# Kernel optimization log

Measured on AMD Instinct MI355X. Metric: run time of the kernel, lower is better.

The kernel has to match this reference:

```python
import jax, jax.numpy as jnp
import numpy as np

NEG = 0.01  # LeakyReLU negative_slope
N_NODES = 100000
N_EDGES = 400000
D = 128
IN_CH = 16
EDGE_DIM = 1


def _linear(x, w, b):
    # torch.nn.Linear convention: y = x @ W^T + b, W: [out, in]
    return x @ w.T + b


def setup_inputs() -> dict:
    key = jax.random.key(0)
    ks = jax.random.split(key, 32)

    def W(k, o, i):
        return jax.random.normal(k, (o, i), dtype=jnp.float32) * 0.02

    def B(k, o):
        return jax.random.normal(k, (o,), dtype=jnp.float32) * 0.02

    return {
        "x": jax.random.normal(ks[0], (N_NODES, IN_CH), dtype=jnp.float32),
        "edge_index": jax.random.randint(ks[1], (2, N_EDGES), 0, N_NODES, dtype=jnp.int64),
        "edge_weight": jax.random.uniform(ks[2], (N_EDGES, EDGE_DIM), dtype=jnp.float32),
        # prep MLP: in_ch -> 128 (LeakyReLU) -> 128 (Tanh)
        "prep_w0": W(ks[3], D, IN_CH), "prep_b0": B(ks[4], D),
        "prep_w1": W(ks[5], D, D), "prep_b1": B(ks[6], D),
        # GINEConv edge lin: edge_dim -> 128
        "edge_w": W(ks[7], D, EDGE_DIM), "edge_b": B(ks[8], D),
        # GINEConv nn: 128 -> 128 (LReLU) -> 128 (LReLU) -> 128 (Tanh)
        "mlp_w0": W(ks[9], D, D), "mlp_b0": B(ks[10], D),
        "mlp_w1": W(ks[11], D, D), "mlp_b1": B(ks[12], D),
        "mlp_w2": W(ks[13], D, D), "mlp_b2": B(ks[14], D),
        # post MLP: (128+128) -> 128 (LReLU) -> 64 (Tanh)
        "post_w0": W(ks[15], D, 2 * D), "post_b0": B(ks[16], D),
        "post_w1": W(ks[17], 64, D), "post_b1": B(ks[18], 64),
    }


def reference(x, edge_index, edge_weight,
              prep_w0, prep_b0, prep_w1, prep_b1,
              edge_w, edge_b,
              mlp_w0, mlp_b0, mlp_w1, mlp_b1, mlp_w2, mlp_b2,
              post_w0, post_b0, post_w1, post_b1):
    lrelu = lambda v: jax.nn.leaky_relu(v, negative_slope=NEG)
    n = x.shape[0]

    # sequential_prep
    h = lrelu(_linear(x, prep_w0, prep_b0))
    h = jnp.tanh(_linear(h, prep_w1, prep_b1))  # [N, D]

    r = h  # skip connection (x.clone())

    # GINEConv: message = relu(x_j + lin(edge_attr)); aggr = sum per dst
    e = _linear(edge_weight, edge_w, edge_b)            # [E, D]
    m = jax.nn.relu(h[edge_index[0]] + e)               # gather + edge add
    agg = jax.ops.segment_sum(m, edge_index[1], num_segments=n)  # scatter-sum
    z = h + agg  # (1 + eps) * x_i + aggr, eps = 0
    z = lrelu(_linear(z, mlp_w0, mlp_b0))
    z = lrelu(_linear(z, mlp_w1, mlp_b1))
    z = jnp.tanh(_linear(z, mlp_w2, mlp_b2))            # [N, D]

    # skip-cat
    h2 = jnp.concatenate([z, r], axis=1)                # [N, 2D]

    # sequential_post
    o = lrelu(_linear(h2, post_w0, post_b0))
    o = jnp.tanh(_linear(o, post_w1, post_b1))          # [N, 64]
    return o
```

## Files before the change

### kernel.cpp

```cpp
#include <hip/hip_runtime.h>

typedef short bf16x8 __attribute__((ext_vector_type(8)));
typedef float f32x4 __attribute__((ext_vector_type(4)));

#define NEG 0.01f

#define OFF_P0  0
#define OFF_P1  8192
#define OFF_M0  40960
#define OFF_Q0A 139264
#define OFF_Q0B 172032
#define OFF_Q1  204800
#define WBF_BYTES 221184

#define VMCNT0 asm volatile("s_waitcnt vmcnt(0)" ::: "memory")
#define LGKM0  asm volatile("s_waitcnt lgkmcnt(0)" ::: "memory")

__device__ __forceinline__ unsigned short f2bf(float f) {
  union { float f; unsigned u; } v; v.f = f;
  unsigned u = v.u;
  return (unsigned short)((u + 0x7fffu + ((u >> 16) & 1u)) >> 16);
}
__device__ __forceinline__ unsigned pack2(float a, float b) {
  return ((unsigned)f2bf(b) << 16) | (unsigned)f2bf(a);
}
__device__ __forceinline__ float bflo(unsigned u) { return __uint_as_float(u << 16); }
__device__ __forceinline__ float bfhi(unsigned u) { return __uint_as_float(u & 0xffff0000u); }
__device__ __forceinline__ float lrelu(float v) { return fmaxf(v, 0.0f) + NEG * fminf(v, 0.0f); }
__device__ __forceinline__ float tanh_fast(float x) {
  float e = __expf(2.0f * x);
  return 1.0f - __fdividef(2.0f, e + 1.0f);
}

__device__ __forceinline__ void gll16(const void* g, void* l) {
  __builtin_amdgcn_global_load_lds((const __attribute__((address_space(1))) void*)g,
                                   (__attribute__((address_space(3))) void*)l, 16, 0, 0);
}

__device__ __forceinline__ void gll_lin(const char* g, char* l, int nchunks, int wv, int nw, int lane) {
  for (int j = wv; j < nchunks; j += nw)
    gll16(g + j * 1024 + lane * 16, l + j * 1024 + lane * 16);
}

__device__ __forceinline__ void gll_rows(const char* gsrc, char* scr, int strip, int N, int lane) {
  #pragma unroll
  for (int c = 0; c < 8; ++c) {
    int L = c * 1024 + lane * 16;
    int row = strip + (L >> 8);
    row = row < N ? row : N - 1;
    gll16(gsrc + (size_t)row * 256 + (L & 255), scr + c * 1024 + lane * 16);
  }
}

__device__ __forceinline__ void copy_rows_out(const char* scr, char* gdst, int strip, int N, int lane) {
  #pragma unroll
  for (int c = 0; c < 8; ++c) {
    int L = c * 1024 + lane * 16;
    int row = strip + (L >> 8);
    if (row < N) *(uint4*)(gdst + (size_t)strip * 256 + L) = *(const uint4*)(scr + L);
  }
}

__device__ __forceinline__ void zacc82(f32x4 acc[8][2]) {
  #pragma unroll
  for (int m = 0; m < 8; ++m)
    #pragma unroll
    for (int n = 0; n < 2; ++n) { f32x4 z = {0.f,0.f,0.f,0.f}; acc[m][n] = z; }
}

__device__ __forceinline__ void gemm128(const char* wbase, const bf16x8 b[2][4],
                                        f32x4 acc[8][2], int l15, int lg) {
  #pragma unroll
  for (int ks = 0; ks < 4; ++ks)
    #pragma unroll
    for (int mf = 0; mf < 8; ++mf) {
      const int row = 16*mf + l15;
      bf16x8 a = *(const bf16x8*)(wbase + row*256 + ((16*lg + 64*ks) ^ ((row&7)<<4)));
      acc[mf][0] = __builtin_amdgcn_mfma_f32_16x16x32_bf16(a, b[0][ks], acc[mf][0], 0,0,0);
      acc[mf][1] = __builtin_amdgcn_mfma_f32_16x16x32_bf16(a, b[1][ks], acc[mf][1], 0,0,0);
    }
}

__device__ __forceinline__ void read_bfrags(const char* scr, bf16x8 b[2][4], int l15, int lg) {
  #pragma unroll
  for (int nf = 0; nf < 2; ++nf) {
    const int n = 16*nf + l15;
    #pragma unroll
    for (int ks = 0; ks < 4; ++ks)
      b[nf][ks] = *(const bf16x8*)(scr + n*256 + ((16*lg + 64*ks) ^ ((n&7)<<4)));
  }
}

template<int ACT>
__device__ __forceinline__ void ep_lds(const f32x4 acc[8][2], const float* __restrict__ bias,
                                       char* scr, int l15, int lg) {
  #pragma unroll
  for (int mf = 0; mf < 8; ++mf) {
    const int ch4 = 16*mf + 4*lg;
    const float4 bv = *(const float4*)(bias + ch4);
    #pragma unroll
    for (int nf = 0; nf < 2; ++nf) {
      const int n = 16*nf + l15;
      float v0 = acc[mf][nf][0]+bv.x, v1 = acc[mf][nf][1]+bv.y;
      float v2 = acc[mf][nf][2]+bv.z, v3 = acc[mf][nf][3]+bv.w;
      if (ACT == 0) { v0=lrelu(v0); v1=lrelu(v1); v2=lrelu(v2); v3=lrelu(v3); }
      else { v0=tanh_fast(v0); v1=tanh_fast(v1); v2=tanh_fast(v2); v3=tanh_fast(v3); }
      uint2 o = { pack2(v0,v1), pack2(v2,v3) };
      *(uint2*)(scr + n*256 + ((32*mf + 8*lg) ^ ((n&7)<<4))) = o;
    }
  }
}

extern "C" __global__ void __launch_bounds__(256) wpack_kernel(
    const float* __restrict__ pw0, const float* __restrict__ pw1,
    const float* __restrict__ mw0, const float* __restrict__ mw1, const float* __restrict__ mw2,
    const float* __restrict__ qw0, const float* __restrict__ qw1,
    char* wbf, int* deg, int N) {
  int gid = blockIdx.x * 256 + threadIdx.x;
  if (gid < 13824) {
    int c = gid;
    const float* src = nullptr;
    int dstB = 0;
    bool zero = false;
    if (c < 512) { int r = c >> 2, q = c & 3;
      dstB = OFF_P0 + r*64 + ((q*16) ^ ((r&3)<<4));
      if (q < 2) src = pw0 + r*16 + q*8; else zero = true;
    } else if (c < 2560) { int i = c - 512, r = i >> 4, q = i & 15;
      dstB = OFF_P1 + r*256 + ((q*16) ^ ((r&7)<<4));
      src = pw1 + r*128 + q*8;
    } else if (c < 8704) { int i = c - 2560, sl = i >> 11, j = i & 2047, r = j >> 4, q = j & 15;
      const float* m = (sl==0) ? mw0 : ((sl==1) ? mw1 : mw2);
      dstB = OFF_M0 + sl*32768 + r*256 + ((q*16) ^ ((r&7)<<4));
      src = m + r*128 + q*8;
    } else if (c < 10752) { int i = c - 8704, r = i >> 4, q = i & 15;
      dstB = OFF_Q0A + r*256 + ((q*16) ^ ((r&7)<<4));
      src = qw0 + r*256 + q*8;
    } else if (c < 12800) { int i = c - 10752, r = i >> 4, q = i & 15;
      dstB = OFF_Q0B + r*256 + ((q*16) ^ ((r&7)<<4));
      src = qw0 + r*256 + 128 + q*8;
    } else { int i = c - 12800, r = i >> 4, q = i & 15;
      dstB = OFF_Q1 + r*256 + ((q*16) ^ ((r&7)<<4));
      src = qw1 + r*128 + q*8;
    }
    ushort4 lo, hi;
    if (zero) { lo.x=lo.y=lo.z=lo.w=0; hi.x=hi.y=hi.z=hi.w=0; }
    else {
      float4 a = *(const float4*)src, b = *(const float4*)(src + 4);
      lo.x=f2bf(a.x); lo.y=f2bf(a.y); lo.z=f2bf(a.z); lo.w=f2bf(a.w);
      hi.x=f2bf(b.x); hi.y=f2bf(b.y); hi.z=f2bf(b.z); hi.w=f2bf(b.w);
    }
    *(ushort4*)(wbf + dstB) = lo;
    *(ushort4*)(wbf + dstB + 8) = hi;
  }
  if (gid < N) deg[gid] = 0;
}

extern "C" __global__ void __launch_bounds__(512) prep_kernel(
    const float* __restrict__ x,
    const float* __restrict__ pb0, const float* __restrict__ pb1,
    const char* __restrict__ wbf,
    const int* __restrict__ ei, int* deg, int E,
    char* hB, int N, int ntiles) {
  __shared__ char wP[40960];
  __shared__ char xw_all[8 * 2048];
  __shared__ char scr_all[8 * 8192];
  const int tid = threadIdx.x, lane = tid & 63, wv = tid >> 6;
  const int l15 = lane & 15, lg = lane >> 4;

  gll_lin(wbf + OFF_P0, wP, 40, wv, 8, lane);
  for (int e = blockIdx.x*512 + tid; e < E; e += gridDim.x*512)
    atomicAdd(&deg[ei[E + e]], 1);
  VMCNT0; __syncthreads();

  char* xw  = xw_all  + wv * 2048;
  char* scr = scr_all + wv * 8192;
  const char* xc = (const char*)x;

  for (int tile = blockIdx.x; tile < ntiles; tile += gridDim.x) {
    const int strip = tile*256 + wv*32;
    LGKM0;
    #pragma unroll
    for (int c = 0; c < 2; ++c) {
      int L = c*1024 + lane*16;
      int row = strip + (L >> 6);
      row = row < N ? row : N - 1;
      gll16(xc + (size_t)row*64 + (L & 63), xw + c*1024 + lane*16);
    }
    VMCNT0;
    bf16x8 bx[2];
    #pragma unroll
    for (int nf = 0; nf < 2; ++nf) {
      const int n = 16*nf + l15;
      if (lg < 2) {
        float4 u = *(const float4*)(xw + n*64 + lg*32);
        float4 v = *(const float4*)(xw + n*64 + lg*32 + 16);
        bf16x8 t;
        t[0]=(short)f2bf(u.x); t[1]=(short)f2bf(u.y); t[2]=(short)f2bf(u.z); t[3]=(short)f2bf(u.w);
        t[4]=(short)f2bf(v.x); t[5]=(short)f2bf(v.y); t[6]=(short)f2bf(v.z); t[7]=(short)f2bf(v.w);
        bx[nf] = t;
      } else {
        bf16x8 t = {0,0,0,0,0,0,0,0}; bx[nf] = t;
      }
    }
    f32x4 acc[8][2];
    zacc82(acc);
    #pragma unroll
    for (int mf = 0; mf < 8; ++mf) {
      const int row = 16*mf + l15;
      bf16x8 a = *(const bf16x8*)(wP + row*64 + ((16*lg) ^ ((row&3)<<4)));
      acc[mf][0] = __builtin_amdgcn_mfma_f32_16x16x32_bf16(a, bx[0], acc[mf][0], 0,0,0);
      acc[mf][1] = __builtin_amdgcn_mfma_f32_16x16x32_bf16(a, bx[1], acc[mf][1], 0,0,0);
    }
    ep_lds<0>(acc, pb0, scr, l15, lg);
    bf16x8 b1[2][4];
    read_bfrags(scr, b1, l15, lg);
    zacc82(acc);
    gemm128(wP + 8192, b1, acc, l15, lg);
    ep_lds<1>(acc, pb1, scr, l15, lg);
    copy_rows_out(scr, hB, strip, N, lane);
  }
}

extern "C" __global__ void __launch_bounds__(256) scan_partials_kernel(
    const int* __restrict__ deg, int* partials, int N) {
  __shared__ int red[256];
  int b = blockIdx.x, t = threadIdx.x;
  int base = b * 2048 + t * 8, s = 0;
  #pragma unroll
  for (int i = 0; i < 8; ++i) { int idx = base + i; s += (idx < N) ? deg[idx] : 0; }
  red[t] = s; __syncthreads();
  for (int off = 128; off > 0; off >>= 1) {
    if (t < off) red[t] += red[t + off];
    __syncthreads();
  }
  if (t == 0) partials[b] = red[0];
}

extern "C" __global__ void scan_base_kernel(const int* __restrict__ partials, int* basearr, int nb) {
  int lane = threadIdx.x;
  int orig = (lane < nb) ? partials[lane] : 0;
  int v = orig;
  #pragma unroll
  for (int off = 1; off < 64; off <<= 1) {
    int u = __shfl_up(v, off);
    if (lane >= off) v += u;
  }
  if (lane < nb) basearr[lane] = v - orig;
}

extern "C" __global__ void __launch_bounds__(256) scan_apply_kernel(
    const int* __restrict__ deg, const int* __restrict__ basearr,
    int* offs, int* cur, int N) {
  __shared__ int sc[256];
  int b = blockIdx.x, t = threadIdx.x;
  int base = b * 2048 + t * 8;
  int loc[8], s = 0;
  #pragma unroll
  for (int i = 0; i < 8; ++i) { int idx = base + i; loc[i] = (idx < N) ? deg[idx] : 0; s += loc[i]; }
  sc[t] = s; __syncthreads();
  for (int off = 1; off < 256; off <<= 1) {
    int v = sc[t];
    int u = (t >= off) ? sc[t - off] : 0;
    __syncthreads();
    sc[t] = v + u;
    __syncthreads();
  }
  int run = basearr[b] + ((t == 0) ? 0 : sc[t - 1]);
  #pragma unroll
  for (int i = 0; i < 8; ++i) {
    int idx = base + i;
    if (idx < N) { offs[idx] = run; cur[idx] = run; run += loc[i]; }
  }
}

extern "C" __global__ void __launch_bounds__(256) scatter_kernel(
    const int* __restrict__ ei, const float* __restrict__ ew,
    int* cur, int2* recs, int E) {
  int e = blockIdx.x * 256 + threadIdx.x;
  if (e < E) {
    int dst = ei[E + e];
    int slot = atomicAdd(&cur[dst], 1);
    int2 r; r.x = ei[e]; r.y = __float_as_int(ew[e]);
    recs[slot] = r;
  }
}

extern "C" __global__ void __launch_bounds__(256) agg_kernel(
    const int* __restrict__ offs, const int* __restrict__ cur,
    const int2* __restrict__ recs,
    const float* __restrict__ elw, const float* __restrict__ elb,
    const char* __restrict__ hB, char* zB, int N) {
  const int lane = threadIdx.x & 63, wv = threadIdx.x >> 6;
  const int node = blockIdx.x * 4 + wv;
  if (node >= N) return;
  const float2 wl = *(const float2*)(elw + 2*lane);
  const float2 bl = *(const float2*)(elb + 2*lane);
  const int byteL = lane * 4;
  const int s = offs[node], e = cur[node];
  float c0 = 0.f, c1 = 0.f;
  int j = s;
  for (; j + 4 <= e; j += 4) {
    int2 r0 = recs[j], r1 = recs[j+1], r2 = recs[j+2], r3 = recs[j+3];
    unsigned u0 = *(const unsigned*)(hB + (size_t)r0.x*256 + (byteL ^ ((r0.x&7)<<4)));
    unsigned u1 = *(const unsigned*)(hB + (size_t)r1.x*256 + (byteL ^ ((r1.x&7)<<4)));
    unsigned u2 = *(const unsigned*)(hB + (size_t)r2.x*256 + (byteL ^ ((r2.x&7)<<4)));
    unsigned u3 = *(const unsigned*)(hB + (size_t)r3.x*256 + (byteL ^ ((r3.x&7)<<4)));
    float w0 = __int_as_float(r0.y), w1 = __int_as_float(r1.y);
    float w2 = __int_as_float(r2.y), w3 = __int_as_float(r3.y);
    c0 += fmaxf(bflo(u0) + w0*wl.x + bl.x, 0.f); c1 += fmaxf(bfhi(u0) + w0*wl.y + bl.y, 0.f);
    c0 += fmaxf(bflo(u1) + w1*wl.x + bl.x, 0.f); c1 += fmaxf(bfhi(u1) + w1*wl.y + bl.y, 0.f);
    c0 += fmaxf(bflo(u2) + w2*wl.x + bl.x, 0.f); c1 += fmaxf(bfhi(u2) + w2*wl.y + bl.y, 0.f);
    c0 += fmaxf(bflo(u3) + w3*wl.x + bl.x, 0.f); c1 += fmaxf(bfhi(u3) + w3*wl.y + bl.y, 0.f);
  }
  for (; j < e; ++j) {
    int2 r = recs[j];
    unsigned u = *(const unsigned*)(hB + (size_t)r.x*256 + (byteL ^ ((r.x&7)<<4)));
    float w = __int_as_float(r.y);
    c0 += fmaxf(bflo(u) + w*wl.x + bl.x, 0.f);
    c1 += fmaxf(bfhi(u) + w*wl.y + bl.y, 0.f);
  }
  unsigned hs = *(const unsigned*)(hB + (size_t)node*256 + (byteL ^ ((node&7)<<4)));
  unsigned o = pack2(bflo(hs) + c0, bfhi(hs) + c1);
  *(unsigned*)(zB + (size_t)node*256 + (byteL ^ ((node&7)<<4))) = o;
}

extern "C" __global__ void __launch_bounds__(384) nodeA_kernel(
    const char* __restrict__ zB, const char* __restrict__ wbf,
    const float* __restrict__ mb0, const float* __restrict__ mb1, const float* __restrict__ mb2,
    char* z3, int N, int ntiles) {
  __shared__ char wM[98304];
  __shared__ char scrA[6 * 8192];
  const int tid = threadIdx.x, lane = tid & 63, wv = tid >> 6;
  const int l15 = lane & 15, lg = lane >> 4;

  gll_lin(wbf + OFF_M0, wM, 96, wv, 6, lane);
  VMCNT0; __syncthreads();
  char* scr = scrA + wv * 8192;

  for (int tile = blockIdx.x; tile < ntiles; tile += gridDim.x) {
    const int strip = tile*192 + wv*32;
    LGKM0;
    gll_rows(zB, scr, strip, N, lane);
    VMCNT0;
    bf16x8 b0[2][4];
    read_bfrags(scr, b0, l15, lg);
    f32x4 acc[8][2];
    zacc82(acc);
    gemm128(wM, b0, acc, l15, lg);
    ep_lds<0>(acc, mb0, scr, l15, lg);
    bf16x8 b1[2][4];
    read_bfrags(scr, b1, l15, lg);
    zacc82(acc);
    gemm128(wM + 32768, b1, acc, l15, lg);
    ep_lds<0>(acc, mb1, scr, l15, lg);
    bf16x8 b2[2][4];
    read_bfrags(scr, b2, l15, lg);
    zacc82(acc);
    gemm128(wM + 65536, b2, acc, l15, lg);
    ep_lds<1>(acc, mb2, scr, l15, lg);
    copy_rows_out(scr, z3, strip, N, lane);
  }
}

extern "C" __global__ void __launch_bounds__(384) nodeB_kernel(
    const char* __restrict__ z3, const char* __restrict__ hB, const char* __restrict__ wbf,
    const float* __restrict__ qb0, const float* __restrict__ qb1,
    float* out, int N, int ntiles) {
  __shared__ char wQ[81920];
  __shared__ char scrB[6 * 8192];
  const int tid = threadIdx.x, lane = tid & 63, wv = tid >> 6;
  const int l15 = lane & 15, lg = lane >> 4;

  gll_lin(wbf + OFF_Q0A, wQ, 80, wv, 6, lane);
  VMCNT0; __syncthreads();
  char* scr = scrB + wv * 8192;

  for (int tile = blockIdx.x; tile < ntiles; tile += gridDim.x) {
    const int strip = tile*192 + wv*32;
    LGKM0;
    gll_rows(z3, scr, strip, N, lane);
    VMCNT0;
    bf16x8 bz[2][4];
    read_bfrags(scr, bz, l15, lg);
    LGKM0;
    gll_rows(hB, scr, strip, N, lane);
    f32x4 acc[8][2];
    zacc82(acc);
    gemm128(wQ, bz, acc, l15, lg);
    VMCNT0;
    bf16x8 bh[2][4];
    read_bfrags(scr, bh, l15, lg);
    gemm128(wQ + 32768, bh, acc, l15, lg);
    ep_lds<0>(acc, qb0, scr, l15, lg);
    bf16x8 bt[2][4];
    read_bfrags(scr, bt, l15, lg);
    f32x4 a2[4][2];
    #pragma unroll
    for (int m = 0; m < 4; ++m)
      #pragma unroll
      for (int n = 0; n < 2; ++n) { f32x4 z = {0.f,0.f,0.f,0.f}; a2[m][n] = z; }
    #pragma unroll
    for (int ks = 0; ks < 4; ++ks)
      #pragma unroll
      for (int mf = 0; mf < 4; ++mf) {
        const int row = 16*mf + l15;
        bf16x8 a = *(const bf16x8*)(wQ + 65536 + row*256 + ((16*lg + 64*ks) ^ ((row&7)<<4)));
        a2[mf][0] = __builtin_amdgcn_mfma_f32_16x16x32_bf16(a, bt[0][ks], a2[mf][0], 0,0,0);
        a2[mf][1] = __builtin_amdgcn_mfma_f32_16x16x32_bf16(a, bt[1][ks], a2[mf][1], 0,0,0);
      }
    #pragma unroll
    for (int mf = 0; mf < 4; ++mf) {
      const int ch4 = 16*mf + 4*lg;
      const float4 bv = *(const float4*)(qb1 + ch4);
      #pragma unroll
      for (int nf = 0; nf < 2; ++nf) {
        const int node = strip + 16*nf + l15;
        if (node < N) {
          float4 o;
          o.x = tanh_fast(a2[mf][nf][0] + bv.x);
          o.y = tanh_fast(a2[mf][nf][1] + bv.y);
          o.z = tanh_fast(a2[mf][nf][2] + bv.z);
          o.w = tanh_fast(a2[mf][nf][3] + bv.w);
          *(float4*)(out + (size_t)node*64 + ch4) = o;
        }
      }
    }
  }
}

extern "C" void kernel_launch(void* const* d_in, const int* in_sizes, int n_in,
                              void* d_out, int out_size, void* d_ws, size_t ws_size,
                              hipStream_t stream) {
  const float* x   = (const float*)d_in[0];
  const int*   ei  = (const int*)d_in[1];
  const float* ew  = (const float*)d_in[2];
  const float* pw0 = (const float*)d_in[3];
  const float* pb0 = (const float*)d_in[4];
  const float* pw1 = (const float*)d_in[5];
  const float* pb1 = (const float*)d_in[6];
  const float* elw = (const float*)d_in[7];
  const float* elb = (const float*)d_in[8];
  const float* mw0 = (const float*)d_in[9];
  const float* mb0 = (const float*)d_in[10];
  const float* mw1 = (const float*)d_in[11];
  const float* mb1 = (const float*)d_in[12];
  const float* mw2 = (const float*)d_in[13];
  const float* mb2 = (const float*)d_in[14];
  const float* qw0 = (const float*)d_in[15];
  const float* qb0 = (const float*)d_in[16];
  const float* qw1 = (const float*)d_in[17];
  const float* qb1 = (const float*)d_in[18];
  float* out = (float*)d_out;

  const int N = in_sizes[0] / 16;
  const int E = in_sizes[1] / 2;

  char* p = (char*)d_ws;
  auto alloc = [&](size_t bytes) { char* r = p; p += (bytes + 255) & ~(size_t)255; return r; };
  const size_t rowBytes = (size_t)N * 256;

  char* zB      = alloc(rowBytes);
  char* z3      = alloc(rowBytes);
  int2* recs    = (int2*)alloc((size_t)E * 8);
  int*  deg     = (int*)alloc((size_t)N * 4);
  int*  offs    = (int*)alloc((size_t)N * 4);
  int*  cur     = (int*)alloc((size_t)N * 4);
  int*  part    = (int*)alloc(256 * 4);
  int*  basearr = (int*)alloc(256 * 4);
  char* wbf     = alloc(WBF_BYTES);

  char* hB;
  if ((size_t)(p - (char*)d_ws) + rowBytes <= ws_size) {
    hB = alloc(rowBytes);
  } else {
    hB = (char*)d_out;
  }

  const int ntilesP  = (N + 255) / 256;
  const int ntilesAB = (N + 191) / 192;
  const int nb1  = (N + 2047) / 2048;
  const int eblk = (E + 255) / 256;
  const int pgrid = ((13824 > N ? 13824 : N) + 255) / 256;

  wpack_kernel<<<dim3(pgrid), dim3(256), 0, stream>>>(pw0, pw1, mw0, mw1, mw2, qw0, qw1,
                                                      wbf, deg, N);
  prep_kernel<<<dim3(256), dim3(512), 0, stream>>>(x, pb0, pb1, wbf, ei, deg, E, hB, N, ntilesP);
  scan_partials_kernel<<<dim3(nb1), dim3(256), 0, stream>>>(deg, part, N);
  scan_base_kernel<<<dim3(1), dim3(64), 0, stream>>>(part, basearr, nb1);
  scan_apply_kernel<<<dim3(nb1), dim3(256), 0, stream>>>(deg, basearr, offs, cur, N);
  scatter_kernel<<<dim3(eblk), dim3(256), 0, stream>>>(ei, ew, cur, recs, E);
  agg_kernel<<<dim3((N + 3) / 4), dim3(256), 0, stream>>>(offs, cur, recs, elw, elb, hB, zB, N);
  nodeA_kernel<<<dim3(256), dim3(384), 0, stream>>>(zB, wbf, mb0, mb1, mb2, z3, N, ntilesAB);
  nodeB_kernel<<<dim3(256), dim3(384), 0, stream>>>(z3, hB, wbf, qb0, qb1, out, N, ntilesAB);
}
```

Baseline: 278.5 us.

## Fuse node MLP kernels, single-block CSR scan, read weights from global

Merges nodeA and nodeB into one node kernel so the z3 intermediate is never written to or read back from global memory. The three scan kernels are replaced by one 1024-thread single-block scan. The prep and node kernels now use one 256-node tile per block instead of persistent loops, and read weight fragments straight from global/L2 instead of staging them in LDS. This frees LDS for two blocks per CU, at the cost of repeated global weight reads and a serial single-block scan.

```diff
diff --git a/kernel.cpp b/kernel.cpp
--- a/kernel.cpp
+++ b/kernel.cpp
@@ -14,7 +14,6 @@
 #define WBF_BYTES 221184
 
 #define VMCNT0 asm volatile("s_waitcnt vmcnt(0)" ::: "memory")
-#define LGKM0  asm volatile("s_waitcnt lgkmcnt(0)" ::: "memory")
 
 __device__ __forceinline__ unsigned short f2bf(float f) {
   union { float f; unsigned u; } v; v.f = f;
@@ -35,11 +34,6 @@
 __device__ __forceinline__ void gll16(const void* g, void* l) {
   __builtin_amdgcn_global_load_lds((const __attribute__((address_space(1))) void*)g,
                                    (__attribute__((address_space(3))) void*)l, 16, 0, 0);
-}
-
-__device__ __forceinline__ void gll_lin(const char* g, char* l, int nchunks, int wv, int nw, int lane) {
-  for (int j = wv; j < nchunks; j += nw)
-    gll16(g + j * 1024 + lane * 16, l + j * 1024 + lane * 16);
 }
 
 __device__ __forceinline__ void gll_rows(const char* gsrc, char* scr, int strip, int N, int lane) {
@@ -155,121 +149,88 @@
   if (gid < N) deg[gid] = 0;
 }
 
-extern "C" __global__ void __launch_bounds__(512) prep_kernel(
+extern "C" __global__ void __launch_bounds__(512, 2) prep_kernel(
     const float* __restrict__ x,
     const float* __restrict__ pb0, const float* __restrict__ pb1,
     const char* __restrict__ wbf,
     const int* __restrict__ ei, int* deg, int E,
-    char* hB, int N, int ntiles) {
-  __shared__ char wP[40960];
-  __shared__ char xw_all[8 * 2048];
+    char* hB, int N) {
   __shared__ char scr_all[8 * 8192];
   const int tid = threadIdx.x, lane = tid & 63, wv = tid >> 6;
   const int l15 = lane & 15, lg = lane >> 4;
-
-  gll_lin(wbf + OFF_P0, wP, 40, wv, 8, lane);
+  char* scr = scr_all + wv * 8192;
+
   for (int e = blockIdx.x*512 + tid; e < E; e += gridDim.x*512)
     atomicAdd(&deg[ei[E + e]], 1);
-  VMCNT0; __syncthreads();
-
-  char* xw  = xw_all  + wv * 2048;
-  char* scr = scr_all + wv * 8192;
-  const char* xc = (const char*)x;
-
-  for (int tile = blockIdx.x; tile < ntiles; tile += gridDim.x) {
-    const int strip = tile*256 + wv*32;
-    LGKM0;
-    #pragma unroll
-    for (int c = 0; c < 2; ++c) {
-      int L = c*1024 + lane*16;
-      int row = strip + (L >> 6);
-      row = row < N ? row : N - 1;
-      gll16(xc + (size_t)row*64 + (L & 63), xw + c*1024 + lane*16);
-    }
-    VMCNT0;
-    bf16x8 bx[2];
-    #pragma unroll
-    for (int nf = 0; nf < 2; ++nf) {
-      const int n = 16*nf + l15;
-      if (lg < 2) {
-        float4 u = *(const float4*)(xw + n*64 + lg*32);
-        float4 v = *(const float4*)(xw + n*64 + lg*32 + 16);
-        bf16x8 t;
-        t[0]=(short)f2bf(u.x); t[1]=(short)f2bf(u.y); t[2]=(short)f2bf(u.z); t[3]=(short)f2bf(u.w);
-        t[4]=(short)f2bf(v.x); t[5]=(short)f2bf(v.y); t[6]=(short)f2bf(v.z); t[7]=(short)f2bf(v.w);
-        bx[nf] = t;
-      } else {
-        bf16x8 t = {0,0,0,0,0,0,0,0}; bx[nf] = t;
-      }
-    }
-    f32x4 acc[8][2];
-    zacc82(acc);
-    #pragma unroll
-    for (int mf = 0; mf < 8; ++mf) {
-      const int row = 16*mf + l15;
-      bf16x8 a = *(const bf16x8*)(wP + row*64 + ((16*lg) ^ ((row&3)<<4)));
-      acc[mf][0] = __builtin_amdgcn_mfma_f32_16x16x32_bf16(a, bx[0], acc[mf][0], 0,0,0);
-      acc[mf][1] = __builtin_amdgcn_mfma_f32_16x16x32_bf16(a, bx[1], acc[mf][1], 0,0,0);
-    }
-    ep_lds<0>(acc, pb0, scr, l15, lg);
-    bf16x8 b1[2][4];
-    read_bfrags(scr, b1, l15, lg);
-    zacc82(acc);
-    gemm128(wP + 8192, b1, acc, l15, lg);
-    ep_lds<1>(acc, pb1, scr, l15, lg);
-    copy_rows_out(scr, hB, strip, N, lane);
-  }
-}
-
-extern "C" __global__ void __launch_bounds__(256) scan_partials_kernel(
-    const int* __restrict__ deg, int* partials, int N) {
-  __shared__ int red[256];
-  int b = blockIdx.x, t = threadIdx.x;
-  int base = b * 2048 + t * 8, s = 0;
-  #pragma unroll
-  for (int i = 0; i < 8; ++i) { int idx = base + i; s += (idx < N) ? deg[idx] : 0; }
-  red[t] = s; __syncthreads();
-  for (int off = 128; off > 0; off >>= 1) {
-    if (t < off) red[t] += red[t + off];
+
+  const int strip = blockIdx.x*256 + wv*32;
+  if (strip >= N) return;
+
+  bf16x8 bx[2];
+  #pragma unroll
+  for (int nf = 0; nf < 2; ++nf) {
+    int node = strip + 16*nf + l15; node = node < N ? node : N-1;
+    if (lg < 2) {
+      float4 u = *(const float4*)(x + (size_t)node*16 + lg*8);
+      float4 v = *(const float4*)(x + (size_t)node*16 + lg*8 + 4);
+      bf16x8 t;
+      t[0]=(short)f2bf(u.x); t[1]=(short)f2bf(u.y); t[2]=(short)f2bf(u.z); t[3]=(short)f2bf(u.w);
+      t[4]=(short)f2bf(v.x); t[5]=(short)f2bf(v.y); t[6]=(short)f2bf(v.z); t[7]=(short)f2bf(v.w);
+      bx[nf] = t;
+    } else {
+      bf16x8 t = {0,0,0,0,0,0,0,0}; bx[nf] = t;
+    }
+  }
+  f32x4 acc[8][2];
+  zacc82(acc);
+  #pragma unroll
+  for (int mf = 0; mf < 8; ++mf) {
+    const int row = 16*mf + l15;
+    bf16x8 a = *(const bf16x8*)(wbf + OFF_P0 + row*64 + ((16*lg) ^ ((row&3)<<4)));
+    acc[mf][0] = __builtin_amdgcn_mfma_f32_16x16x32_bf16(a, bx[0], acc[mf][0], 0,0,0);
+    acc[mf][1] = __builtin_amdgcn_mfma_f32_16x16x32_bf16(a, bx[1], acc[mf][1], 0,0,0);
+  }
+  ep_lds<0>(acc, pb0, scr, l15, lg);
+  bf16x8 b1[2][4];
+  read_bfrags(scr, b1, l15, lg);
+  zacc82(acc);
+  gemm128(wbf + OFF_P1, b1, acc, l15, lg);
+  ep_lds<1>(acc, pb1, scr, l15, lg);
+  copy_rows_out(scr, hB, strip, N, lane);
+}
+
+extern "C" __global__ void __launch_bounds__(1024) csr_kernel(
+    const int* __restrict__ deg, int* offs, int* cur, int N) {
+  __shared__ int sums[1024];
+  const int t = threadIdx.x;
+  const int i0 = t * 128;
+  int s = 0;
+  if (i0 < N) {
+    int lim = (i0 + 128 < N) ? i0 + 128 : N;
+    int i = i0;
+    for (; i + 4 <= lim; i += 4) { int4 d = *(const int4*)(deg + i); s += d.x + d.y + d.z + d.w; }
+    for (; i < lim; ++i) s += deg[i];
+  }
+  sums[t] = s;
+  __syncthreads();
+  for (int off = 1; off < 1024; off <<= 1) {
+    int v = sums[t];
+    int u = (t >= off) ? sums[t - off] : 0;
     __syncthreads();
-  }
-  if (t == 0) partials[b] = red[0];
-}
-
-extern "C" __global__ void scan_base_kernel(const int* __restrict__ partials, int* basearr, int nb) {
-  int lane = threadIdx.x;
-  int orig = (lane < nb) ? partials[lane] : 0;
-  int v = orig;
-  #pragma unroll
-  for (int off = 1; off < 64; off <<= 1) {
-    int u = __shfl_up(v, off);
-    if (lane >= off) v += u;
-  }
-  if (lane < nb) basearr[lane] = v - orig;
-}
-
-extern "C" __global__ void __launch_bounds__(256) scan_apply_kernel(
-    const int* __restrict__ deg, const int* __restrict__ basearr,
-    int* offs, int* cur, int N) {
-  __shared__ int sc[256];
-  int b = blockIdx.x, t = threadIdx.x;
-  int base = b * 2048 + t * 8;
-  int loc[8], s = 0;
-  #pragma unroll
-  for (int i = 0; i < 8; ++i) { int idx = base + i; loc[i] = (idx < N) ? deg[idx] : 0; s += loc[i]; }
-  sc[t] = s; __syncthreads();
-  for (int off = 1; off < 256; off <<= 1) {
-    int v = sc[t];
-    int u = (t >= off) ? sc[t - off] : 0;
+    sums[t] = v + u;
     __syncthreads();
-    sc[t] = v + u;
-    __syncthreads();
-  }
-  int run = basearr[b] + ((t == 0) ? 0 : sc[t - 1]);
-  #pragma unroll
-  for (int i = 0; i < 8; ++i) {
-    int idx = base + i;
-    if (idx < N) { offs[idx] = run; cur[idx] = run; run += loc[i]; }
+  }
+  int run = (t == 0) ? 0 : sums[t - 1];
+  if (i0 < N) {
+    int lim = (i0 + 128 < N) ? i0 + 128 : N;
+    int i = i0;
+    for (; i + 4 <= lim; i += 4) {
+      int4 d = *(const int4*)(deg + i);
+      int4 o; o.x = run; o.y = run + d.x; o.z = o.y + d.y; o.w = o.z + d.z;
+      *(int4*)(offs + i) = o; *(int4*)(cur + i) = o;
+      run = o.w + d.w;
+    }
+    for (; i < lim; ++i) { offs[i] = run; cur[i] = run; run += deg[i]; }
   }
 }
 
@@ -324,105 +285,88 @@
   *(unsigned*)(zB + (size_t)node*256 + (byteL ^ ((node&7)<<4))) = o;
 }
 
-extern "C" __global__ void __launch_bounds__(384) nodeA_kernel(
-    const char* __restrict__ zB, const char* __restrict__ wbf,
+extern "C" __global__ void __launch_bounds__(512, 2) node_kernel(
+    const char* __restrict__ zB, const char* hB, const char* __restrict__ wbf,
     const float* __restrict__ mb0, const float* __restrict__ mb1, const float* __restrict__ mb2,
-    char* z3, int N, int ntiles) {
-  __shared__ char wM[98304];
-  __shared__ char scrA[6 * 8192];
+    const float* __restrict__ qb0, const float* __restrict__ qb1,
+    float* out, int N) {
+  __shared__ char scr_all[8 * 8192];
   const int tid = threadIdx.x, lane = tid & 63, wv = tid >> 6;
   const int l15 = lane & 15, lg = lane >> 4;
-
-  gll_lin(wbf + OFF_M0, wM, 96, wv, 6, lane);
-  VMCNT0; __syncthreads();
-  char* scr = scrA + wv * 8192;
-
-  for (int tile = blockIdx.x; tile < ntiles; tile += gridDim.x) {
-    const int strip = tile*192 + wv*32;
-    LGKM0;
-    gll_rows(zB, scr, strip, N, lane);
-    VMCNT0;
-    bf16x8 b0[2][4];
-    read_bfrags(scr, b0, l15, lg);
-    f32x4 acc[8][2];
-    zacc82(acc);
-    gemm128(wM, b0, acc, l15, lg);
-    ep_lds<0>(acc, mb0, scr, l15, lg);
-    bf16x8 b1[2][4];
-    read_bfrags(scr, b1, l15, lg);
-    zacc82(acc);
-    gemm128(wM + 32768, b1, acc, l15, lg);
-    ep_lds<0>(acc, mb1, scr, l15, lg);
-    bf16x8 b2[2][4];
-    read_bfrags(scr, b2, l15, lg);
-    zacc82(acc);
-    gemm128(wM + 65536, b2, acc, l15, lg);
-    ep_lds<1>(acc, mb2, scr, l15, lg);
-    copy_rows_out(scr, z3, strip, N, lane);
-  }
-}
-
-extern "C" __global__ void __launch_bounds__(384) nodeB_kernel(
-    const char* __restrict__ z3, const char* __restrict__ hB, const char* __restrict__ wbf,
-    const float* __restrict__ qb0, const float* __restrict__ qb1,
-    float* out, int N, int ntiles) {
-  __shared__ char wQ[81920];
-  __shared__ char scrB[6 * 8192];
-  const int tid = threadIdx.x, lane = tid & 63, wv = tid >> 6;
-  const int l15 = lane & 15, lg = lane >> 4;
-
-  gll_lin(wbf + OFF_Q0A, wQ, 80, wv, 6, lane);
-  VMCNT0; __syncthreads();
-  char* scr = scrB + wv * 8192;
-
-  for (int tile = blockIdx.x; tile < ntiles; tile += gridDim.x) {
-    const int strip = tile*192 + wv*32;
-    LGKM0;
-    gll_rows(z3, scr, strip, N, lane);
-    VMCNT0;
-    bf16x8 bz[2][4];
-    read_bfrags(scr, bz, l15, lg);
-    LGKM0;
-    gll_rows(hB, scr, strip, N, lane);
-    f32x4 acc[8][2];
-    zacc82(acc);
-    gemm128(wQ, bz, acc, l15, lg);
-    VMCNT0;
-    bf16x8 bh[2][4];
-    read_bfrags(scr, bh, l15, lg);
-    gemm128(wQ + 32768, bh, acc, l15, lg);
-    ep_lds<0>(acc, qb0, scr, l15, lg);
-    bf16x8 bt[2][4];
-    read_bfrags(scr, bt, l15, lg);
-    f32x4 a2[4][2];
-    #pragma unroll
-    for (int m = 0; m < 4; ++m)
-      #pragma unroll
-      for (int n = 0; n < 2; ++n) { f32x4 z = {0.f,0.f,0.f,0.f}; a2[m][n] = z; }
+  char* scr = scr_all + wv * 8192;
+
+  const int strip = blockIdx.x*256 + wv*32;
+  if (strip >= N) return;
+
+  gll_rows(zB, scr, strip, N, lane);
+  VMCNT0;
+
+  bf16x8 b0[2][4];
+  read_bfrags(scr, b0, l15, lg);
+  f32x4 acc[8][2];
+  zacc82(acc);
+  gemm128(wbf + OFF_M0, b0, acc, l15, lg);
+  ep_lds<0>(acc, mb0, scr, l15, lg);
+
+  bf16x8 b1[2][4];
+  read_bfrags(scr, b1, l15, lg);
+  zacc82(acc);
+  gemm128(wbf + OFF_M0 + 32768, b1, acc, l15, lg);
+  ep_lds<0>(acc, mb1, scr, l15, lg);
+
+  bf16x8 b2[2][4];
+  read_bfrags(scr, b2, l15, lg);
+  zacc82(acc);
+  gemm128(wbf + OFF_M0 + 65536, b2, acc, l15, lg);
+  ep_lds<1>(acc, mb2, scr, l15, lg);
+
+  bf16x8 bz[2][4];
+  read_bfrags(scr, bz, l15, lg);
+  bf16x8 bh[2][4];
+  #pragma unroll
+  for (int nf = 0; nf < 2; ++nf) {
+    int node = strip + 16*nf + l15; node = node < N ? node : N-1;
+    const char* hr = hB + (size_t)node*256;
+    const int sw = (node&7) << 4;
     #pragma unroll
     for (int ks = 0; ks < 4; ++ks)
-      #pragma unroll
-      for (int mf = 0; mf < 4; ++mf) {
-        const int row = 16*mf + l15;
-        bf16x8 a = *(const bf16x8*)(wQ + 65536 + row*256 + ((16*lg + 64*ks) ^ ((row&7)<<4)));
-        a2[mf][0] = __builtin_amdgcn_mfma_f32_16x16x32_bf16(a, bt[0][ks], a2[mf][0], 0,0,0);
-        a2[mf][1] = __builtin_amdgcn_mfma_f32_16x16x32_bf16(a, bt[1][ks], a2[mf][1], 0,0,0);
-      }
+      bh[nf][ks] = *(const bf16x8*)(hr + ((16*lg + 64*ks) ^ sw));
+  }
+  zacc82(acc);
+  gemm128(wbf + OFF_Q0A, bz, acc, l15, lg);
+  gemm128(wbf + OFF_Q0B, bh, acc, l15, lg);
+  ep_lds<0>(acc, qb0, scr, l15, lg);
+
+  bf16x8 bt[2][4];
+  read_bfrags(scr, bt, l15, lg);
+  f32x4 a2[4][2];
+  #pragma unroll
+  for (int m = 0; m < 4; ++m)
+    #pragma unroll
+    for (int n = 0; n < 2; ++n) { f32x4 z = {0.f,0.f,0.f,0.f}; a2[m][n] = z; }
+  #pragma unroll
+  for (int ks = 0; ks < 4; ++ks)
     #pragma unroll
     for (int mf = 0; mf < 4; ++mf) {
-      const int ch4 = 16*mf + 4*lg;
-      const float4 bv = *(const float4*)(qb1 + ch4);
-      #pragma unroll
-      for (int nf = 0; nf < 2; ++nf) {
-        const int node = strip + 16*nf + l15;
-        if (node < N) {
-          float4 o;
-          o.x = tanh_fast(a2[mf][nf][0] + bv.x);
-          o.y = tanh_fast(a2[mf][nf][1] + bv.y);
-          o.z = tanh_fast(a2[mf][nf][2] + bv.z);
-          o.w = tanh_fast(a2[mf][nf][3] + bv.w);
-          *(float4*)(out + (size_t)node*64 + ch4) = o;
-        }
+      const int row = 16*mf + l15;
+      bf16x8 a = *(const bf16x8*)(wbf + OFF_Q1 + row*256 + ((16*lg + 64*ks) ^ ((row&7)<<4)));
+      a2[mf][0] = __builtin_amdgcn_mfma_f32_16x16x32_bf16(a, bt[0][ks], a2[mf][0], 0,0,0);
+      a2[mf][1] = __builtin_amdgcn_mfma_f32_16x16x32_bf16(a, bt[1][ks], a2[mf][1], 0,0,0);
+    }
+  #pragma unroll
+  for (int mf = 0; mf < 4; ++mf) {
+    const int ch4 = 16*mf + 4*lg;
+    const float4 bv = *(const float4*)(qb1 + ch4);
+    #pragma unroll
+    for (int nf = 0; nf < 2; ++nf) {
+      const int node = strip + 16*nf + l15;
+      if (node < N) {
+        float4 o;
+        o.x = tanh_fast(a2[mf][nf][0] + bv.x);
+        o.y = tanh_fast(a2[mf][nf][1] + bv.y);
+        o.z = tanh_fast(a2[mf][nf][2] + bv.z);
+        o.w = tanh_fast(a2[mf][nf][3] + bv.w);
+        *(float4*)(out + (size_t)node*64 + ch4) = o;
       }
     }
   }
@@ -460,13 +404,10 @@
   const size_t rowBytes = (size_t)N * 256;
 
   char* zB      = alloc(rowBytes);
-  char* z3      = alloc(rowBytes);
   int2* recs    = (int2*)alloc((size_t)E * 8);
   int*  deg     = (int*)alloc((size_t)N * 4);
   int*  offs    = (int*)alloc((size_t)N * 4);
   int*  cur     = (int*)alloc((size_t)N * 4);
-  int*  part    = (int*)alloc(256 * 4);
-  int*  basearr = (int*)alloc(256 * 4);
   char* wbf     = alloc(WBF_BYTES);
 
   char* hB;
@@ -476,20 +417,16 @@
     hB = (char*)d_out;
   }
 
-  const int ntilesP  = (N + 255) / 256;
-  const int ntilesAB = (N + 191) / 192;
-  const int nb1  = (N + 2047) / 2048;
+  const int nblk = (N + 255) / 256;
   const int eblk = (E + 255) / 256;
   const int pgrid = ((13824 > N ? 13824 : N) + 255) / 256;
 
   wpack_kernel<<<dim3(pgrid), dim3(256), 0, stream>>>(pw0, pw1, mw0, mw1, mw2, qw0, qw1,
                                                       wbf, deg, N);
-  prep_kernel<<<dim3(256), dim3(512), 0, stream>>>(x, pb0, pb1, wbf, ei, deg, E, hB, N, ntilesP);
-  scan_partials_kernel<<<dim3(nb1), dim3(256), 0, stream>>>(deg, part, N);
-  scan_base_kernel<<<dim3(1), dim3(64), 0, stream>>>(part, basearr, nb1);
-  scan_apply_kernel<<<dim3(nb1), dim3(256), 0, stream>>>(deg, basearr, offs, cur, N);
+  prep_kernel<<<dim3(nblk), dim3(512), 0, stream>>>(x, pb0, pb1, wbf, ei, deg, E, hB, N);
+  csr_kernel<<<dim3(1), dim3(1024), 0, stream>>>(deg, offs, cur, N);
   scatter_kernel<<<dim3(eblk), dim3(256), 0, stream>>>(ei, ew, cur, recs, E);
   agg_kernel<<<dim3((N + 3) / 4), dim3(256), 0, stream>>>(offs, cur, recs, elw, elb, hB, zB, N);
-  nodeA_kernel<<<dim3(256), dim3(384), 0, stream>>>(zB, wbf, mb0, mb1, mb2, z3, N, ntilesAB);
-  nodeB_kernel<<<dim3(256), dim3(384), 0, stream>>>(z3, hB, wbf, qb0, qb1, out, N, ntilesAB);
-}
+  node_kernel<<<dim3(nblk), dim3(512), 0, stream>>>(zB, hB, wbf, mb0, mb1, mb2,
+                                                    qb0, qb1, out, N);
+}
```

Result: slower. 345.6 us (+24.1%).

## Widen node kernels, load inputs directly to registers, add MFMA priority hints

Applied to the files above, without the earlier changes.

The node MLP kernels get more waves per block (7 and 8 instead of 6) with larger tiles, so the per-block weight loads are spread over more rows. The prep kernel reads x straight into registers instead of staging it through LDS, and nodeB loads the skip features hB directly from global into B fragments rather than through a second LDS staging pass. s_setprio hints are placed around the MFMA loops, and the LGKM waits are removed. The larger blocks may reduce occupancy or leave the last tiles underfilled, and the direct global loads give up the coalesced LDS staging.

```diff
diff --git a/kernel.cpp b/kernel.cpp
--- a/kernel.cpp
+++ b/kernel.cpp
@@ -14,7 +14,6 @@
 #define WBF_BYTES 221184
 
 #define VMCNT0 asm volatile("s_waitcnt vmcnt(0)" ::: "memory")
-#define LGKM0  asm volatile("s_waitcnt lgkmcnt(0)" ::: "memory")
 
 __device__ __forceinline__ unsigned short f2bf(float f) {
   union { float f; unsigned u; } v; v.f = f;
@@ -70,6 +69,7 @@
 
 __device__ __forceinline__ void gemm128(const char* wbase, const bf16x8 b[2][4],
                                         f32x4 acc[8][2], int l15, int lg) {
+  __builtin_amdgcn_s_setprio(1);
   #pragma unroll
   for (int ks = 0; ks < 4; ++ks)
     #pragma unroll
@@ -79,6 +79,7 @@
       acc[mf][0] = __builtin_amdgcn_mfma_f32_16x16x32_bf16(a, b[0][ks], acc[mf][0], 0,0,0);
       acc[mf][1] = __builtin_amdgcn_mfma_f32_16x16x32_bf16(a, b[1][ks], acc[mf][1], 0,0,0);
     }
+  __builtin_amdgcn_s_setprio(0);
 }
 
 __device__ __forceinline__ void read_bfrags(const char* scr, bf16x8 b[2][4], int l15, int lg) {
@@ -162,7 +163,6 @@
     const int* __restrict__ ei, int* deg, int E,
     char* hB, int N, int ntiles) {
   __shared__ char wP[40960];
-  __shared__ char xw_all[8 * 2048];
   __shared__ char scr_all[8 * 8192];
   const int tid = threadIdx.x, lane = tid & 63, wv = tid >> 6;
   const int l15 = lane & 15, lg = lane >> 4;
@@ -171,29 +171,18 @@
   for (int e = blockIdx.x*512 + tid; e < E; e += gridDim.x*512)
     atomicAdd(&deg[ei[E + e]], 1);
   VMCNT0; __syncthreads();
-
-  char* xw  = xw_all  + wv * 2048;
   char* scr = scr_all + wv * 8192;
-  const char* xc = (const char*)x;
 
   for (int tile = blockIdx.x; tile < ntiles; tile += gridDim.x) {
     const int strip = tile*256 + wv*32;
-    LGKM0;
-    #pragma unroll
-    for (int c = 0; c < 2; ++c) {
-      int L = c*1024 + lane*16;
-      int row = strip + (L >> 6);
-      row = row < N ? row : N - 1;
-      gll16(xc + (size_t)row*64 + (L & 63), xw + c*1024 + lane*16);
-    }
-    VMCNT0;
+    if (strip >= N) continue;
     bf16x8 bx[2];
     #pragma unroll
     for (int nf = 0; nf < 2; ++nf) {
-      const int n = 16*nf + l15;
+      int node = strip + 16*nf + l15; node = node < N ? node : N-1;
       if (lg < 2) {
-        float4 u = *(const float4*)(xw + n*64 + lg*32);
-        float4 v = *(const float4*)(xw + n*64 + lg*32 + 16);
+        float4 u = *(const float4*)(x + (size_t)node*16 + lg*8);
+        float4 v = *(const float4*)(x + (size_t)node*16 + lg*8 + 4);
         bf16x8 t;
         t[0]=(short)f2bf(u.x); t[1]=(short)f2bf(u.y); t[2]=(short)f2bf(u.z); t[3]=(short)f2bf(u.w);
         t[4]=(short)f2bf(v.x); t[5]=(short)f2bf(v.y); t[6]=(short)f2bf(v.z); t[7]=(short)f2bf(v.w);
@@ -204,6 +193,7 @@
     }
     f32x4 acc[8][2];
     zacc82(acc);
+    __builtin_amdgcn_s_setprio(1);
     #pragma unroll
     for (int mf = 0; mf < 8; ++mf) {
       const int row = 16*mf + l15;
@@ -211,6 +201,7 @@
       acc[mf][0] = __builtin_amdgcn_mfma_f32_16x16x32_bf16(a, bx[0], acc[mf][0], 0,0,0);
       acc[mf][1] = __builtin_amdgcn_mfma_f32_16x16x32_bf16(a, bx[1], acc[mf][1], 0,0,0);
     }
+    __builtin_amdgcn_s_setprio(0);
     ep_lds<0>(acc, pb0, scr, l15, lg);
     bf16x8 b1[2][4];
     read_bfrags(scr, b1, l15, lg);
@@ -324,22 +315,22 @@
   *(unsigned*)(zB + (size_t)node*256 + (byteL ^ ((node&7)<<4))) = o;
 }
 
-extern "C" __global__ void __launch_bounds__(384) nodeA_kernel(
+extern "C" __global__ void __launch_bounds__(448) nodeA_kernel(
     const char* __restrict__ zB, const char* __restrict__ wbf,
     const float* __restrict__ mb0, const float* __restrict__ mb1, const float* __restrict__ mb2,
     char* z3, int N, int ntiles) {
   __shared__ char wM[98304];
-  __shared__ char scrA[6 * 8192];
+  __shared__ char scr_all[7 * 8192];
   const int tid = threadIdx.x, lane = tid & 63, wv = tid >> 6;
   const int l15 = lane & 15, lg = lane >> 4;
 
-  gll_lin(wbf + OFF_M0, wM, 96, wv, 6, lane);
+  gll_lin(wbf + OFF_M0, wM, 96, wv, 7, lane);
   VMCNT0; __syncthreads();
-  char* scr = scrA + wv * 8192;
+  char* scr = scr_all + wv * 8192;
 
   for (int tile = blockIdx.x; tile < ntiles; tile += gridDim.x) {
-    const int strip = tile*192 + wv*32;
-    LGKM0;
+    const int strip = tile*224 + wv*32;
+    if (strip >= N) continue;
     gll_rows(zB, scr, strip, N, lane);
     VMCNT0;
     bf16x8 b0[2][4];
@@ -362,36 +353,42 @@
   }
 }
 
-extern "C" __global__ void __launch_bounds__(384) nodeB_kernel(
-    const char* __restrict__ z3, const char* __restrict__ hB, const char* __restrict__ wbf,
+extern "C" __global__ void __launch_bounds__(512) nodeB_kernel(
+    const char* __restrict__ z3, const char* hB, const char* __restrict__ wbf,
     const float* __restrict__ qb0, const float* __restrict__ qb1,
     float* out, int N, int ntiles) {
   __shared__ char wQ[81920];
-  __shared__ char scrB[6 * 8192];
+  __shared__ char scr_all[8 * 8192];
   const int tid = threadIdx.x, lane = tid & 63, wv = tid >> 6;
   const int l15 = lane & 15, lg = lane >> 4;
 
-  gll_lin(wbf + OFF_Q0A, wQ, 80, wv, 6, lane);
+  gll_lin(wbf + OFF_Q0A, wQ, 80, wv, 8, lane);
   VMCNT0; __syncthreads();
-  char* scr = scrB + wv * 8192;
+  char* scr = scr_all + wv * 8192;
 
   for (int tile = blockIdx.x; tile < ntiles; tile += gridDim.x) {
-    const int strip = tile*192 + wv*32;
-    LGKM0;
+    const int strip = tile*256 + wv*32;
+    if (strip >= N) continue;
     gll_rows(z3, scr, strip, N, lane);
+    bf16x8 bh[2][4];
+    #pragma unroll
+    for (int nf = 0; nf < 2; ++nf) {
+      int node = strip + 16*nf + l15; node = node < N ? node : N-1;
+      const char* hr = hB + (size_t)node*256;
+      const int sw = (node&7) << 4;
+      #pragma unroll
+      for (int ks = 0; ks < 4; ++ks)
+        bh[nf][ks] = *(const bf16x8*)(hr + ((16*lg + 64*ks) ^ sw));
+    }
     VMCNT0;
     bf16x8 bz[2][4];
     read_bfrags(scr, bz, l15, lg);
-    LGKM0;
-    gll_rows(hB, scr, strip, N, lane);
     f32x4 acc[8][2];
     zacc82(acc);
     gemm128(wQ, bz, acc, l15, lg);
-    VMCNT0;
-    bf16x8 bh[2][4];
-    read_bfrags(scr, bh, l15, lg);
     gemm128(wQ + 32768, bh, acc, l15, lg);
     ep_lds<0>(acc, qb0, scr, l15, lg);
+
     bf16x8 bt[2][4];
     read_bfrags(scr, bt, l15, lg);
     f32x4 a2[4][2];
@@ -399,6 +396,7 @@
     for (int m = 0; m < 4; ++m)
       #pragma unroll
       for (int n = 0; n < 2; ++n) { f32x4 z = {0.f,0.f,0.f,0.f}; a2[m][n] = z; }
+    __builtin_amdgcn_s_setprio(1);
     #pragma unroll
     for (int ks = 0; ks < 4; ++ks)
       #pragma unroll
@@ -408,6 +406,7 @@
         a2[mf][0] = __builtin_amdgcn_mfma_f32_16x16x32_bf16(a, bt[0][ks], a2[mf][0], 0,0,0);
         a2[mf][1] = __builtin_amdgcn_mfma_f32_16x16x32_bf16(a, bt[1][ks], a2[mf][1], 0,0,0);
       }
+    __builtin_amdgcn_s_setprio(0);
     #pragma unroll
     for (int mf = 0; mf < 4; ++mf) {
       const int ch4 = 16*mf + 4*lg;
@@ -476,8 +475,9 @@
     hB = (char*)d_out;
   }
 
-  const int ntilesP  = (N + 255) / 256;
-  const int ntilesAB = (N + 191) / 192;
+  const int ntilesP = (N + 255) / 256;
+  const int ntilesA = (N + 223) / 224;
+  const int ntilesB = (N + 255) / 256;
   const int nb1  = (N + 2047) / 2048;
   const int eblk = (E + 255) / 256;
   const int pgrid = ((13824 > N ? 13824 : N) + 255) / 256;
@@ -490,6 +490,6 @@
   scan_apply_kernel<<<dim3(nb1), dim3(256), 0, stream>>>(deg, basearr, offs, cur, N);
   scatter_kernel<<<dim3(eblk), dim3(256), 0, stream>>>(ei, ew, cur, recs, E);
   agg_kernel<<<dim3((N + 3) / 4), dim3(256), 0, stream>>>(offs, cur, recs, elw, elb, hB, zB, N);
-  nodeA_kernel<<<dim3(256), dim3(384), 0, stream>>>(zB, wbf, mb0, mb1, mb2, z3, N, ntilesAB);
-  nodeB_kernel<<<dim3(256), dim3(384), 0, stream>>>(z3, hB, wbf, qb0, qb1, out, N, ntilesAB);
-}
+  nodeA_kernel<<<dim3(256), dim3(448), 0, stream>>>(zB, wbf, mb0, mb1, mb2, z3, N, ntilesA);
+  nodeB_kernel<<<dim3(256), dim3(512), 0, stream>>>(z3, hB, wbf, qb0, qb1, out, N, ntilesB);
+}
```

After: 259.3 us. 6.9% less time.
